# Optimization experiments

Hardware: AMD Instinct MI355X
Metric: run time of the kernel (lower is better)

The kernel has to match this reference:

```python
import jax, jax.numpy as jnp
import numpy as np

N, C, H, M = 4096, 1024, 16, 4096
D = C // H
EPS = 1e-6


def rms_norm(x, g):
    # RMSNorm32: normalize in fp32 with eps=1e-6, affine scale g
    x32 = x.astype(jnp.float32)
    inv = jax.lax.rsqrt(jnp.mean(x32 * x32, axis=-1, keepdims=True) + EPS)
    return (x32 * inv).astype(x.dtype) * g


def setup_inputs() -> dict:
    key = jax.random.key(0)
    ks = jax.random.split(key, 6)
    s = 1.0 / np.sqrt(C)
    return {
        "x": jax.random.normal(ks[0], (N, C), jnp.float32),
        "g1": jnp.ones((C,), jnp.float32),
        "g2": jnp.ones((C,), jnp.float32),
        "w_qkv": jax.random.normal(ks[1], (C, 3 * C), jnp.float32) * s,
        "w_o": jax.random.normal(ks[2], (C, C), jnp.float32) * s,
        "w1": jax.random.normal(ks[3], (C, M), jnp.float32) * s,
        "w2": jax.random.normal(ks[4], (M, C), jnp.float32) * (1.0 / np.sqrt(M)),
    }


def reference(x, g1, g2, w_qkv, w_o, w1, w2):
    # --- pre-norm + full multi-head self-attention over all N sparse tokens ---
    h = rms_norm(x, g1)                                   # [N, C]
    qkv = (h @ w_qkv).reshape(N, 3, H, D)                 # [N, 3, H, D]
    q, k, v = qkv[:, 0], qkv[:, 1], qkv[:, 2]             # [N, H, D]
    scale = 1.0 / np.sqrt(D)
    scores = jnp.einsum('nhd,mhd->hnm', q, k) * scale     # [H, N, N]
    attn = jax.nn.softmax(scores, axis=-1)
    o = jnp.einsum('hnm,mhd->nhd', attn, v).reshape(N, C) # [N, C]
    x = x + o @ w_o                                       # residual
    # --- pre-norm + gated-free MLP (GELU tanh) ---
    h2 = rms_norm(x, g2)
    m = jax.nn.gelu(h2 @ w1, approximate=True) @ w2       # [N, C]
    return x + m
```

## Files before the change

### kernel.cpp

```cpp
#include <hip/hip_runtime.h>
#include <stdint.h>

#define TOK 4096
#define CH  1024
#define NH  16
#define HD  64
#define FF  4096

typedef __attribute__((ext_vector_type(8))) short bf16x8;
typedef __attribute__((ext_vector_type(4))) float f32x4;
typedef __attribute__((ext_vector_type(16))) float f32x16;

__device__ __forceinline__ unsigned short f2bf(float f) {
    union { float f; unsigned u; } v; v.f = f;
    unsigned u = v.u;
    u += 0x7fffu + ((u >> 16) & 1u);
    return (unsigned short)(u >> 16);
}

__device__ __forceinline__ unsigned cvtpk(float a, float b) {
    unsigned r;
    asm("v_cvt_pk_bf16_f32 %0, %1, %2" : "=v"(r) : "v"(a), "v"(b));
    return r;
}

__device__ __forceinline__ void load_lds16(const void* g, void* l) {
    __builtin_amdgcn_global_load_lds(
        (const __attribute__((address_space(1))) unsigned int*)g,
        (__attribute__((address_space(3))) unsigned int*)l, 16, 0, 0);
}

template<int N> __device__ __forceinline__ void wait_vm_lgkm0() {
    if constexpr (N == 0)      asm volatile("s_waitcnt vmcnt(0) lgkmcnt(0)" ::: "memory");
    else if constexpr (N == 4) asm volatile("s_waitcnt vmcnt(4) lgkmcnt(0)" ::: "memory");
    else if constexpr (N == 8) asm volatile("s_waitcnt vmcnt(8) lgkmcnt(0)" ::: "memory");
    __builtin_amdgcn_sched_barrier(0);
    __builtin_amdgcn_s_barrier();
}

__device__ __forceinline__ float gelu_tanh(float u) {
    float z = 0.7978845608028654f * (u + 0.044715f * u * u * u);
    float e = __expf(2.0f * z);
    return 0.5f * u * (1.0f + (1.0f - 2.0f / (e + 1.0f)));
}

__global__ __launch_bounds__(256) void wT_kernel(const float* __restrict__ in,
                                                 unsigned short* __restrict__ out,
                                                 int K, int Nn) {
    __shared__ float tile[32][33];
    int k0 = blockIdx.x * 32, n0 = blockIdx.y * 32;
    int t = threadIdx.x, r = t >> 3, c = t & 7;
#pragma unroll
    for (int i = 0; i < 4; i++)
        tile[r][c + 8 * i] = in[(size_t)(k0 + r) * Nn + n0 + c + 8 * i];
    __syncthreads();
#pragma unroll
    for (int i = 0; i < 4; i++)
        out[(size_t)(n0 + r) * K + k0 + c + 8 * i] = f2bf(tile[c + 8 * i][r]);
}

__global__ __launch_bounds__(256) void rms_kernel(const float* __restrict__ x,
                                                  const float* __restrict__ g,
                                                  unsigned short* __restrict__ out) {
    int row = blockIdx.x, t = threadIdx.x;
    const float4* xr = (const float4*)(x + (size_t)row * CH);
    float4 v = xr[t];
    float ss = v.x * v.x + v.y * v.y + v.z * v.z + v.w * v.w;
#pragma unroll
    for (int m = 32; m; m >>= 1) ss += __shfl_xor(ss, m, 64);
    __shared__ float wsum[4];
    if ((t & 63) == 0) wsum[t >> 6] = ss;
    __syncthreads();
    float inv = rsqrtf((wsum[0] + wsum[1] + wsum[2] + wsum[3]) * (1.0f / CH) + 1e-6f);
    float4 gv = ((const float4*)g)[t];
    ushort4 o;
    o.x = f2bf(v.x * inv * gv.x);
    o.y = f2bf(v.y * inv * gv.y);
    o.z = f2bf(v.z * inv * gv.z);
    o.w = f2bf(v.w * inv * gv.w);
    ((ushort4*)(out + (size_t)row * CH))[t] = o;
}

template<int BM, int BN, int EPI>
__global__ __launch_bounds__(256) void gemm_bt(const unsigned short* __restrict__ A,
                                               const unsigned short* __restrict__ Bt,
                                               void* __restrict__ outp,
                                               const float* __restrict__ resid,
                                               int M, int Nn, int K) {
    __shared__ __align__(16) unsigned short ldsA[2][BM * 32];
    __shared__ __align__(16) unsigned short ldsB[2][BN * 32];
    const int t = threadIdx.x, l = t & 63, w = t >> 6;
    const int nbn = Nn / BN;
    const int bid = blockIdx.x, nwg = gridDim.x, cpx = nwg >> 3;
    const int swz = (bid & 7) * cpx + (bid >> 3);
    const int bm = swz / nbn, bn = swz % nbn;
    const int wr = w >> 1, wc = w & 1;
    constexpr int MF = BM / 32, NF = BN / 32;
    const unsigned short* Ag = A + (size_t)bm * BM * K;
    const unsigned short* Bg = Bt + (size_t)bn * BN * K;

    f32x4 acc[MF][NF];
#pragma unroll
    for (int m = 0; m < MF; m++)
#pragma unroll
        for (int n = 0; n < NF; n++) acc[m][n] = {0.f, 0.f, 0.f, 0.f};

    auto stage = [&](int buf, int kt) {
#pragma unroll
        for (int p = 0; p < BM / 64; p++) {
            int c = t + 256 * p;
            load_lds16(Ag + (size_t)(c >> 2) * K + kt * 32 + (c & 3) * 8, &ldsA[buf][c * 8]);
        }
#pragma unroll
        for (int p = 0; p < BN / 64; p++) {
            int c = t + 256 * p;
            load_lds16(Bg + (size_t)(c >> 2) * K + kt * 32 + (c & 3) * 8, &ldsB[buf][c * 8]);
        }
    };

    stage(0, 0);
    __syncthreads();
    const int nkt = K >> 5;
    for (int kt = 0; kt < nkt; kt++) {
        const int buf = kt & 1;
        if (kt + 1 < nkt) stage(buf ^ 1, kt + 1);
        bf16x8 af[MF], bfr[NF];
#pragma unroll
        for (int m = 0; m < MF; m++)
            af[m] = *(const bf16x8*)&ldsA[buf][(wr * (BM / 2) + m * 16 + (l & 15)) * 32 + (l >> 4) * 8];
#pragma unroll
        for (int n = 0; n < NF; n++)
            bfr[n] = *(const bf16x8*)&ldsB[buf][(wc * (BN / 2) + n * 16 + (l & 15)) * 32 + (l >> 4) * 8];
#pragma unroll
        for (int m = 0; m < MF; m++)
#pragma unroll
            for (int n = 0; n < NF; n++)
                acc[m][n] = __builtin_amdgcn_mfma_f32_16x16x32_bf16(af[m], bfr[n], acc[m][n], 0, 0, 0);
        __syncthreads();
    }

    const int r0 = bm * BM + wr * (BM / 2), c0 = bn * BN + wc * (BN / 2);
#pragma unroll
    for (int m = 0; m < MF; m++)
#pragma unroll
        for (int n = 0; n < NF; n++)
#pragma unroll
            for (int r = 0; r < 4; r++) {
                int rr = r0 + m * 16 + (l >> 4) * 4 + r;
                int cc = c0 + n * 16 + (l & 15);
                float v = acc[m][n][r];
                if (EPI == 0) {
                    ((unsigned short*)outp)[(size_t)rr * Nn + cc] = f2bf(v);
                } else if (EPI == 1) {
                    ((unsigned short*)outp)[(size_t)rr * Nn + cc] = f2bf(gelu_tanh(v));
                } else {
                    ((float*)outp)[(size_t)rr * Nn + cc] = resid[(size_t)rr * Nn + cc] + v;
                }
            }
}

template<int EPI>
__global__ __launch_bounds__(512) void gemm256(const unsigned short* __restrict__ A,
                                               const unsigned short* __restrict__ Bt,
                                               void* __restrict__ outp,
                                               unsigned short* __restrict__ vout,
                                               int M, int Nn, int K) {
    __shared__ __align__(16) unsigned short lds[2][4][8192];
    const int t = threadIdx.x, l = t & 63, w = t >> 6;
    const int wr = w >> 2, wc = w & 3;
    const int nbn = Nn >> 8;
    const int bid = blockIdx.x, nwg = gridDim.x, cpx = nwg >> 3;
    const int swz = (bid & 7) * cpx + (bid >> 3);
    const int bm = swz / nbn, bn = swz % nbn;

    const int lbase = (((l & 15) * 64 + (l >> 4) * 16)) ^ (((l >> 3) & 1) << 5);

    int srow[2], scol[2];
#pragma unroll
    for (int L = 0; L < 2; L++) {
        int g = t + L * 512;
        int s = g >> 6;
        int wb = ((g & 63) * 16) ^ (((g >> 5) & 1) << 5);
        srow[L] = (s >> 1) * 16 + (wb >> 6);
        scol[L] = (s & 1) * 32 + ((wb & 63) >> 1);
    }

    const unsigned short* Asrc = A + (size_t)(bm * 256) * K;
    const unsigned short* Bsrc = Bt + (size_t)(bn * 256) * K;

    auto stage_half = [&](int j) {
        const int kt = j >> 2, slot = j & 3;
        const unsigned short* base = (slot < 2 ? Asrc : Bsrc) + (size_t)((slot & 1) * 128) * K;
#pragma unroll
        for (int L = 0; L < 2; L++)
            load_lds16(base + (size_t)srow[L] * K + kt * 64 + scol[L],
                       &lds[kt & 1][slot][(t + L * 512) * 8]);
    };

    f32x4 acc[8][4];
#pragma unroll
    for (int m = 0; m < 8; m++)
#pragma unroll
        for (int n = 0; n < 4; n++) acc[m][n] = {0.f, 0.f, 0.f, 0.f};

    const int nkt = K >> 6;
    stage_half(0); stage_half(1); stage_half(2); stage_half(3);

    for (int kt = 0; kt < nkt; kt++) {
        wait_vm_lgkm0<0>();
        const char* Abase = (const char*)&lds[kt & 1][wr][0];
        const char* Bbase = (const char*)&lds[kt & 1][2 + (wc >> 1)][0];
        bf16x8 bfr[4][2];
#pragma unroll
        for (int q = 0; q < 4; q++) {
            if (q == 0) {
#pragma unroll
                for (int n = 0; n < 4; n++)
#pragma unroll
                    for (int ks = 0; ks < 2; ks++)
                        bfr[n][ks] = *(const bf16x8*)(Bbase + ((((wc & 1) * 4 + n) * 2 + ks) * 1024 + lbase));
            }
            bf16x8 af[2][2];
#pragma unroll
            for (int mi = 0; mi < 2; mi++)
#pragma unroll
                for (int ks = 0; ks < 2; ks++)
                    af[mi][ks] = *(const bf16x8*)(Abase + (((q * 2 + mi) * 2 + ks) * 1024 + lbase));
            if (kt + 1 < nkt) stage_half((kt + 1) * 4 + q);
            __builtin_amdgcn_s_barrier();
            __builtin_amdgcn_s_setprio(1);
#pragma unroll
            for (int mi = 0; mi < 2; mi++)
#pragma unroll
                for (int n = 0; n < 4; n++) {
                    acc[q * 2 + mi][n] = __builtin_amdgcn_mfma_f32_16x16x32_bf16(af[mi][0], bfr[n][0], acc[q * 2 + mi][n], 0, 0, 0);
                    acc[q * 2 + mi][n] = __builtin_amdgcn_mfma_f32_16x16x32_bf16(af[mi][1], bfr[n][1], acc[q * 2 + mi][n], 0, 0, 0);
                }
            __builtin_amdgcn_s_setprio(0);
            __builtin_amdgcn_s_barrier();
        }
    }

    const int r0 = bm * 256 + wr * 128, c0 = bn * 256 + wc * 64;
    const bool vpart = (EPI == 3) && (c0 >= 2048);
#pragma unroll
    for (int m = 0; m < 8; m++)
#pragma unroll
        for (int n = 0; n < 4; n++) {
            if (vpart) {
                int cc = c0 + n * 16 + (l & 15);
                int rrb = r0 + m * 16 + (l >> 4) * 4;
                ushort4 pk;
                pk.x = f2bf(acc[m][n][0]);
                pk.y = f2bf(acc[m][n][1]);
                pk.z = f2bf(acc[m][n][2]);
                pk.w = f2bf(acc[m][n][3]);
                *(ushort4*)(vout + (size_t)(cc - 2048) * 4096 + rrb) = pk;
            } else {
#pragma unroll
                for (int r = 0; r < 4; r++) {
                    int rr = r0 + m * 16 + (l >> 4) * 4 + r;
                    int cc = c0 + n * 16 + (l & 15);
                    float v = acc[m][n][r];
                    if (EPI == 1) {
                        ((unsigned short*)outp)[(size_t)rr * Nn + cc] = f2bf(gelu_tanh(v));
                    } else {
                        float sc = (cc < 1024) ? 0.180336880f : 1.0f;
                        ((unsigned short*)outp)[(size_t)rr * Nn + cc] = f2bf(v * sc);
                    }
                }
            }
        }
}

__global__ __launch_bounds__(256) void attn_kernel(const unsigned short* __restrict__ qkv,
                                                   const unsigned short* __restrict__ vT,
                                                   unsigned short* __restrict__ o) {
    __shared__ __align__(16) unsigned short Kl[3][4096];
    __shared__ __align__(16) unsigned short Vl[3][4096];
    const int t = threadIdx.x, l = t & 63, w = t >> 6;
    const int h = blockIdx.y;
    const int qrow = blockIdx.x * 128 + w * 32 + (l & 31);

    bf16x8 qf[4];
    {
        const unsigned short* qp = qkv + (size_t)qrow * 3072 + h * 64 + ((l >> 5) * 8);
#pragma unroll
        for (int c = 0; c < 4; c++) qf[c] = *(const bf16x8*)(qp + 16 * c);
    }
    const unsigned short* kb = qkv + 1024 + h * 64;
    const unsigned short* vb = vT + (size_t)h * 64 * 4096;

    int off8[4];
#pragma unroll
    for (int c = 0; c < 4; c++)
        off8[c] = (l & 31) * 64 + ((((l >> 5) + 2 * c) ^ (l & 7)) * 8);
    int kst[2], vst[2];
#pragma unroll
    for (int p = 0; p < 2; p++) {
        int c = t + 256 * p;
        int r = c >> 3, b = c & 7;
        kst[p] = r * 3072 + ((b ^ (r & 7)) * 8);
        vst[p] = r * 4096 + ((b ^ (r & 7)) * 8);
    }

    float lrun = 0.f;
    const f32x16 z16 = {0.f, 0.f, 0.f, 0.f, 0.f, 0.f, 0.f, 0.f,
                        0.f, 0.f, 0.f, 0.f, 0.f, 0.f, 0.f, 0.f};
    f32x16 accO[2];
#pragma unroll
    for (int dt = 0; dt < 2; dt++) accO[dt] = z16;

    auto stage = [&](int buf, int kt) {
#pragma unroll
        for (int p = 0; p < 2; p++)
            load_lds16(kb + (size_t)kt * 64 * 3072 + kst[p], &Kl[buf][(t + 256 * p) * 8]);
#pragma unroll
        for (int p = 0; p < 2; p++)
            load_lds16(vb + kt * 64 + vst[p], &Vl[buf][(t + 256 * p) * 8]);
    };

    stage(0, 0);
    stage(1, 1);
    wait_vm_lgkm0<4>();

    for (int kt = 0; kt < 64; kt++) {
        const int cur = kt % 3;
        if (kt + 2 < 64) stage((kt + 2) % 3, kt + 2);

        f32x16 s[2];
        __builtin_amdgcn_s_setprio(1);
#pragma unroll
        for (int st = 0; st < 2; st++) {
            bf16x8 kf0 = *(const bf16x8*)&Kl[cur][st * 2048 + off8[0]];
            s[st] = __builtin_amdgcn_mfma_f32_32x32x16_bf16(kf0, qf[0], z16, 0, 0, 0);
#pragma unroll
            for (int c = 1; c < 4; c++) {
                bf16x8 kf = *(const bf16x8*)&Kl[cur][st * 2048 + off8[c]];
                s[st] = __builtin_amdgcn_mfma_f32_32x32x16_bf16(kf, qf[c], s[st], 0, 0, 0);
            }
        }
        __builtin_amdgcn_s_setprio(0);

        float rs = 0.f;
#pragma unroll
        for (int st = 0; st < 2; st++)
#pragma unroll
            for (int i = 0; i < 16; i++) {
                float p = __builtin_amdgcn_exp2f(s[st][i]);
                s[st][i] = p;
                rs += p;
            }
        lrun += rs;

#pragma unroll
        for (int kc = 0; kc < 4; kc++) {
            const int base = 8 * (kc & 1);
            const f32x16& S = s[kc >> 1];
            unsigned w0 = cvtpk(S[base + 0], S[base + 1]);
            unsigned w1 = cvtpk(S[base + 2], S[base + 3]);
            unsigned w2 = cvtpk(S[base + 4], S[base + 5]);
            unsigned w3 = cvtpk(S[base + 6], S[base + 7]);
            asm("v_permlane32_swap_b32 %0, %1" : "+v"(w0), "+v"(w2));
            asm("v_permlane32_swap_b32 %0, %1" : "+v"(w1), "+v"(w3));
            union { unsigned u[4]; bf16x8 v; } pf;
            pf.u[0] = w0; pf.u[1] = w1; pf.u[2] = w2; pf.u[3] = w3;
            __builtin_amdgcn_s_setprio(1);
#pragma unroll
            for (int dt = 0; dt < 2; dt++) {
                bf16x8 vf = *(const bf16x8*)&Vl[cur][dt * 2048 + off8[kc]];
                accO[dt] = __builtin_amdgcn_mfma_f32_32x32x16_bf16(vf, pf.v, accO[dt], 0, 0, 0);
            }
            __builtin_amdgcn_s_setprio(0);
        }

        if (kt < 63) {
            if (kt + 2 < 64) wait_vm_lgkm0<4>();
            else             wait_vm_lgkm0<0>();
        }
    }

    lrun += __shfl_xor(lrun, 32, 64);
    float inv = 1.0f / lrun;
    unsigned short* ob = o + (size_t)qrow * CH + h * 64 + 4 * (l >> 5);
#pragma unroll
    for (int dt = 0; dt < 2; dt++)
#pragma unroll
        for (int qd = 0; qd < 4; qd++) {
            ushort4 pk;
            pk.x = f2bf(accO[dt][qd * 4 + 0] * inv);
            pk.y = f2bf(accO[dt][qd * 4 + 1] * inv);
            pk.z = f2bf(accO[dt][qd * 4 + 2] * inv);
            pk.w = f2bf(accO[dt][qd * 4 + 3] * inv);
            *(ushort4*)(ob + dt * 32 + qd * 8) = pk;
        }
}

extern "C" void kernel_launch(void* const* d_in, const int* in_sizes, int n_in,
                              void* d_out, int out_size, void* d_ws, size_t ws_size,
                              hipStream_t stream) {
    const float* x     = (const float*)d_in[0];
    const float* g1    = (const float*)d_in[1];
    const float* g2    = (const float*)d_in[2];
    const float* w_qkv = (const float*)d_in[3];
    const float* w_o   = (const float*)d_in[4];
    const float* w1    = (const float*)d_in[5];
    const float* w2    = (const float*)d_in[6];

    char* ws = (char*)d_ws;
    unsigned short* wqkvT = (unsigned short*)(ws);
    unsigned short* woT   = (unsigned short*)(ws + 6291456);
    unsigned short* w1T   = (unsigned short*)(ws + 8388608);
    unsigned short* w2T   = (unsigned short*)(ws + 16777216);
    unsigned short* hbuf  = (unsigned short*)(ws + 25165824);
    unsigned short* qkv   = (unsigned short*)(ws + 33554432);
    unsigned short* obuf  = (unsigned short*)(ws + 58720256);
    float*          x2    = (float*)(ws + 67108864);
    unsigned short* abuf  = (unsigned short*)(ws + 83886080);
    unsigned short* vTb   = (unsigned short*)(ws + 83886080);

    dim3 b256(256), b512(512);
    wT_kernel<<<dim3(CH / 32, 3 * CH / 32), b256, 0, stream>>>(w_qkv, wqkvT, CH, 3 * CH);
    wT_kernel<<<dim3(CH / 32, CH / 32),     b256, 0, stream>>>(w_o,   woT,   CH, CH);
    wT_kernel<<<dim3(CH / 32, FF / 32),     b256, 0, stream>>>(w1,    w1T,   CH, FF);
    wT_kernel<<<dim3(FF / 32, CH / 32),     b256, 0, stream>>>(w2,    w2T,   FF, CH);

    rms_kernel<<<TOK, b256, 0, stream>>>(x, g1, hbuf);
    gemm256<3><<<(TOK / 256) * (3 * CH / 256), b512, 0, stream>>>(hbuf, wqkvT, qkv, vTb, TOK, 3 * CH, CH);
    attn_kernel<<<dim3(TOK / 128, NH), b256, 0, stream>>>(qkv, vTb, obuf);
    gemm_bt<64, 64, 2><<<(TOK / 64) * (CH / 64), b256, 0, stream>>>(obuf, woT, x2, x, TOK, CH, CH);
    rms_kernel<<<TOK, b256, 0, stream>>>(x2, g2, hbuf);
    gemm256<1><<<(TOK / 256) * (FF / 256), b512, 0, stream>>>(hbuf, w1T, abuf, nullptr, TOK, FF, CH);
    gemm_bt<64, 64, 2><<<(TOK / 64) * (CH / 64), b256, 0, stream>>>(abuf, w2T, (float*)d_out, x2, TOK, CH, FF);
}
```

Baseline: 293.7 us.

## Shrink attention blocks to two waves with double buffering; vectorize weight transpose

The attention kernel now uses 128-thread blocks covering 64 query rows instead of 256 threads covering 128. The grid doubles, and each block keeps two K/V stage buffers instead of three, synchronised with plain __syncthreads instead of vmcnt-based waits. This is meant to raise occupancy and shrink LDS per block, at the cost of each thread issuing twice as many staging loads, K/V being reused across fewer query rows, and less prefetch depth since the wait now blocks on the most recent stage. Separately, the weight-transpose kernel switches to float4 loads and ushort4 stores with a padded tile, cutting the number of memory instructions.

```diff
diff --git a/kernel.cpp b/kernel.cpp
--- a/kernel.cpp
+++ b/kernel.cpp
@@ -47,16 +47,19 @@
 __global__ __launch_bounds__(256) void wT_kernel(const float* __restrict__ in,
                                                  unsigned short* __restrict__ out,
                                                  int K, int Nn) {
-    __shared__ float tile[32][33];
+    __shared__ float tile[32][36];
     int k0 = blockIdx.x * 32, n0 = blockIdx.y * 32;
-    int t = threadIdx.x, r = t >> 3, c = t & 7;
-#pragma unroll
-    for (int i = 0; i < 4; i++)
-        tile[r][c + 8 * i] = in[(size_t)(k0 + r) * Nn + n0 + c + 8 * i];
+    int t = threadIdx.x;
+    int r = t >> 3, c4 = (t & 7) * 4;
+    float4 v = *(const float4*)(in + (size_t)(k0 + r) * Nn + n0 + c4);
+    *(float4*)&tile[r][c4] = v;
     __syncthreads();
-#pragma unroll
-    for (int i = 0; i < 4; i++)
-        out[(size_t)(n0 + r) * K + k0 + c + 8 * i] = f2bf(tile[c + 8 * i][r]);
+    ushort4 o;
+    o.x = f2bf(tile[c4 + 0][r]);
+    o.y = f2bf(tile[c4 + 1][r]);
+    o.z = f2bf(tile[c4 + 2][r]);
+    o.w = f2bf(tile[c4 + 3][r]);
+    *(ushort4*)(out + (size_t)(n0 + r) * K + k0 + c4) = o;
 }
 
 __global__ __launch_bounds__(256) void rms_kernel(const float* __restrict__ x,
@@ -273,14 +276,14 @@
         }
 }
 
-__global__ __launch_bounds__(256) void attn_kernel(const unsigned short* __restrict__ qkv,
+__global__ __launch_bounds__(128) void attn_kernel(const unsigned short* __restrict__ qkv,
                                                    const unsigned short* __restrict__ vT,
                                                    unsigned short* __restrict__ o) {
-    __shared__ __align__(16) unsigned short Kl[3][4096];
-    __shared__ __align__(16) unsigned short Vl[3][4096];
+    __shared__ __align__(16) unsigned short Kl[2][4096];
+    __shared__ __align__(16) unsigned short Vl[2][4096];
     const int t = threadIdx.x, l = t & 63, w = t >> 6;
     const int h = blockIdx.y;
-    const int qrow = blockIdx.x * 128 + w * 32 + (l & 31);
+    const int qrow = blockIdx.x * 64 + w * 32 + (l & 31);
 
     bf16x8 qf[4];
     {
@@ -295,10 +298,10 @@
 #pragma unroll
     for (int c = 0; c < 4; c++)
         off8[c] = (l & 31) * 64 + ((((l >> 5) + 2 * c) ^ (l & 7)) * 8);
-    int kst[2], vst[2];
-#pragma unroll
-    for (int p = 0; p < 2; p++) {
-        int c = t + 256 * p;
+    int kst[4], vst[4];
+#pragma unroll
+    for (int p = 0; p < 4; p++) {
+        int c = t + 128 * p;
         int r = c >> 3, b = c & 7;
         kst[p] = r * 3072 + ((b ^ (r & 7)) * 8);
         vst[p] = r * 4096 + ((b ^ (r & 7)) * 8);
@@ -313,20 +316,19 @@
 
     auto stage = [&](int buf, int kt) {
 #pragma unroll
-        for (int p = 0; p < 2; p++)
-            load_lds16(kb + (size_t)kt * 64 * 3072 + kst[p], &Kl[buf][(t + 256 * p) * 8]);
-#pragma unroll
-        for (int p = 0; p < 2; p++)
-            load_lds16(vb + kt * 64 + vst[p], &Vl[buf][(t + 256 * p) * 8]);
+        for (int p = 0; p < 4; p++)
+            load_lds16(kb + (size_t)kt * 64 * 3072 + kst[p], &Kl[buf][(t + 128 * p) * 8]);
+#pragma unroll
+        for (int p = 0; p < 4; p++)
+            load_lds16(vb + kt * 64 + vst[p], &Vl[buf][(t + 128 * p) * 8]);
     };
 
     stage(0, 0);
-    stage(1, 1);
-    wait_vm_lgkm0<4>();
+    __syncthreads();
 
     for (int kt = 0; kt < 64; kt++) {
-        const int cur = kt % 3;
-        if (kt + 2 < 64) stage((kt + 2) % 3, kt + 2);
+        const int cur = kt & 1;
+        if (kt + 1 < 64) stage(cur ^ 1, kt + 1);
 
         f32x16 s[2];
         __builtin_amdgcn_s_setprio(1);
@@ -373,11 +375,7 @@
             }
             __builtin_amdgcn_s_setprio(0);
         }
-
-        if (kt < 63) {
-            if (kt + 2 < 64) wait_vm_lgkm0<4>();
-            else             wait_vm_lgkm0<0>();
-        }
+        __syncthreads();
     }
 
     lrun += __shfl_xor(lrun, 32, 64);
@@ -419,7 +417,7 @@
     unsigned short* abuf  = (unsigned short*)(ws + 83886080);
     unsigned short* vTb   = (unsigned short*)(ws + 83886080);
 
-    dim3 b256(256), b512(512);
+    dim3 b128(128), b256(256), b512(512);
     wT_kernel<<<dim3(CH / 32, 3 * CH / 32), b256, 0, stream>>>(w_qkv, wqkvT, CH, 3 * CH);
     wT_kernel<<<dim3(CH / 32, CH / 32),     b256, 0, stream>>>(w_o,   woT,   CH, CH);
     wT_kernel<<<dim3(CH / 32, FF / 32),     b256, 0, stream>>>(w1,    w1T,   CH, FF);
@@ -427,7 +425,7 @@
 
     rms_kernel<<<TOK, b256, 0, stream>>>(x, g1, hbuf);
     gemm256<3><<<(TOK / 256) * (3 * CH / 256), b512, 0, stream>>>(hbuf, wqkvT, qkv, vTb, TOK, 3 * CH, CH);
-    attn_kernel<<<dim3(TOK / 128, NH), b256, 0, stream>>>(qkv, vTb, obuf);
+    attn_kernel<<<dim3(TOK / 64, NH), b128, 0, stream>>>(qkv, vTb, obuf);
     gemm_bt<64, 64, 2><<<(TOK / 64) * (CH / 64), b256, 0, stream>>>(obuf, woT, x2, x, TOK, CH, CH);
     rms_kernel<<<TOK, b256, 0, stream>>>(x2, g2, hbuf);
     gemm256<1><<<(TOK / 256) * (FF / 256), b512, 0, stream>>>(hbuf, w1T, abuf, nullptr, TOK, FF, CH);
```

Result: slower. 301.2 us (+2.6%).
